# Optimization experiments

Measured on AMD Instinct MI355X. Metric: run time of the kernel, lower is better.

## Reference

```python
import jax, jax.numpy as jnp
import numpy as np

E = 128   # embed_dim / node feature width
H = 4     # num_heads
B = 512   # number of graphs
N = 65536 # total nodes


def setup_inputs() -> dict:
    key = jax.random.key(0)
    ks = jax.random.split(key, 12)
    s = 1.0 / np.sqrt(E)
    batch = jnp.sort(jax.random.randint(ks[0], (N,), 0, B))
    return {
        "x": jax.random.normal(ks[1], (N, E), jnp.float32),
        "metal_x": jax.random.normal(ks[2], (B, E), jnp.float32),
        "batch": batch,
        "Wk": jax.random.normal(ks[3], (E, E), jnp.float32) * s,
        "bk": jnp.zeros((E,), jnp.float32),
        "Wq": jax.random.normal(ks[4], (E, E), jnp.float32) * s,
        "bq": jnp.zeros((E,), jnp.float32),
        "in_w": jax.random.normal(ks[5], (3 * E, E), jnp.float32) * s,
        "in_b": jnp.zeros((3 * E,), jnp.float32),
        "out_w": jax.random.normal(ks[6], (E, E), jnp.float32) * s,
        "out_b": jnp.zeros((E,), jnp.float32),
    }


def reference(x, metal_x, batch, Wk, bk, Wq, bq, in_w, in_b, out_w, out_b):
    n, e = x.shape
    b = metal_x.shape[0]
    nb = np.asarray(batch)
    counts_np = np.bincount(nb, minlength=b)            # nodes per graph
    L = int(counts_np.max()) + 1                        # +1 for metal token at pos 0
    counts = jnp.asarray(counts_np)
    offsets = jnp.asarray(np.concatenate([[0], np.cumsum(counts_np)[:-1]]))
    pos = jnp.arange(n) - offsets[batch] + 1            # within-graph slot (metal at 0)

    # pad_sequence: value [L, B, E], slot 0 = metal_x, slots 1.. = graph nodes
    value = jnp.zeros((L, b, e), x.dtype)
    value = value.at[pos, batch].set(x)
    value = value.at[0, jnp.arange(b)].set(metal_x)

    # FCNN key/query (single hidden linear + relu, no output head)
    k_in = jax.nn.relu(value @ Wk.T + bk)
    q_in = jax.nn.relu(value @ Wq.T + bq)

    # MultiheadAttention (batch_first=False): in_proj then per-head scaled dot-product
    hd = e // H
    q = (q_in @ in_w[:e].T + in_b[:e]).reshape(L, b, H, hd)
    k = (k_in @ in_w[e:2 * e].T + in_b[e:2 * e]).reshape(L, b, H, hd)
    v = (value @ in_w[2 * e:].T + in_b[2 * e:]).reshape(L, b, H, hd)

    scores = jnp.einsum("lbhd,mbhd->bhlm", q, k) * (hd ** -0.5)
    valid = jnp.arange(L)[None, :] < (counts + 1)[:, None]   # [B, L] key_padding mask
    scores = jnp.where(valid[:, None, None, :], scores, jnp.finfo(scores.dtype).min)
    attn = jax.nn.softmax(scores, axis=-1)
    ctx = jnp.einsum("bhlm,mbhd->lbhd", attn, v).reshape(L, b, e)
    out = ctx @ out_w.T + out_b

    x_out = out[pos, batch]      # packed node outputs [N, E]
    metal_out = out[0]           # metal token outputs [B, E]
    return x_out, metal_out
```

## Files before the change

### kernel.cpp

```cpp
#include <hip/hip_runtime.h>

#define E   128
#define HD  32
#define NB  512
#define NN  65536
#define TT  (NB + NN)
#define TE  ((size_t)TT * 128)

typedef __attribute__((ext_vector_type(8))) short short8;
typedef __attribute__((ext_vector_type(4))) float f32x4;

__device__ __forceinline__ const float* row_ptr(const float* base, const float* metal, int t) {
  return (t < NB) ? metal + (size_t)t * E : base + (size_t)(t - NB) * E;
}
__device__ __forceinline__ float* row_ptr_w(float* base, float* metal, int t) {
  return (t < NB) ? metal + (size_t)t * E : base + (size_t)(t - NB) * E;
}

__device__ __forceinline__ unsigned short f2bf_rne(float x) {
  unsigned u = __float_as_uint(x);
  return (unsigned short)((u + 0x7FFFu + ((u >> 16) & 1u)) >> 16);
}
__device__ __forceinline__ void split_bf(float x, unsigned short& h, unsigned short& l) {
  h = f2bf_rne(x);
  float hf = __uint_as_float(((unsigned)h) << 16);
  l = f2bf_rne(x - hf);
}

__global__ void k_starts(const int* __restrict__ batch, int* __restrict__ start) {
  int i = blockIdx.x * blockDim.x + threadIdx.x;
  if (i >= NN) return;
  int bi = batch[i];
  int bp = (i == 0) ? -1 : batch[i - 1];
  for (int b = bp + 1; b <= bi; ++b) start[b] = i;
  if (i == NN - 1)
    for (int b = bi + 1; b <= NB; ++b) start[b] = NN;
}

__global__ void k_seqmap(const int* __restrict__ batch, const int* __restrict__ start,
                         int* __restrict__ seqmap) {
  int t = blockIdx.x * 256 + threadIdx.x;
  if (t >= TT) return;
  seqmap[t] = (t < NB) ? (start[t] + t) : (t - NB + batch[t - NB] + 1);
}

__global__ void k_wconv(const float* __restrict__ Wq, const float* __restrict__ Wk,
                        const float* __restrict__ in_w, const float* __restrict__ out_w,
                        unsigned short* __restrict__ Wh, unsigned short* __restrict__ Wl) {
  int idx = blockIdx.x * 256 + threadIdx.x;
  int r = idx >> 7, c = idx & 127;
  float v;
  if (r < 128)      v = Wq[r * 128 + c];
  else if (r < 256) v = Wk[(r - 128) * 128 + c];
  else if (r < 640) v = in_w[(r - 256) * 128 + c];
  else              v = out_w[(r - 640) * 128 + c];
  unsigned short h, l;
  split_bf(v, h, l);
  Wh[idx] = h;
  Wl[idx] = l;
}

__global__ __launch_bounds__(256, 2)
void k_outproj(const float* __restrict__ Ax, const int* __restrict__ rowmap,
               const unsigned short* __restrict__ Wh, const unsigned short* __restrict__ Wl,
               const float* __restrict__ bias,
               float* __restrict__ Cx, float* __restrict__ Cm) {
  __shared__ char smem[40960];
  float (*Afl)[36] = (float (*)[36])smem;
  unsigned short (*WldsH)[40] = (unsigned short (*)[40])(smem + 20480);
  unsigned short (*WldsL)[40] = (unsigned short (*)[40])(smem + 30720);

  const int tid = threadIdx.x;
  const int wave = tid >> 6;
  const int lane = tid & 63;
  const int lrow = lane & 15;
  const int q = lane >> 4;
  const int t0 = blockIdx.x * 128;

  f32x4 acc[2][8];
  #pragma unroll
  for (int mt = 0; mt < 2; ++mt)
    #pragma unroll
    for (int nt = 0; nt < 8; ++nt) acc[mt][nt] = (f32x4){0.f, 0.f, 0.f, 0.f};

  for (int ks = 0; ks < 4; ++ks) {
    __syncthreads();
    #pragma unroll
    for (int u = 0; u < 4; ++u) {
      int e4 = tid + u * 256;
      int m = e4 >> 3, k4 = e4 & 7;
      const float* rp = Ax + (size_t)rowmap[t0 + m] * E;
      float4 v = ((const float4*)(rp + ks * 32))[k4];
      *(float4*)&Afl[m][k4 * 4] = v;
    }
    #pragma unroll
    for (int u = 0; u < 4; ++u) {
      int idx = tid + u * 256;
      int half = idx >> 9, rem = idx & 511;
      int j = rem >> 2, seg = rem & 3;
      const unsigned short* src = (half ? Wl : Wh) + j * 128 + ks * 32 + seg * 8;
      short8 v = *(const short8*)src;
      unsigned short* dst = (half ? &WldsL[j][seg * 8] : &WldsH[j][seg * 8]);
      *(short8*)dst = v;
    }
    __syncthreads();

    short8 ah[2], al[2];
    #pragma unroll
    for (int mt = 0; mt < 2; ++mt) {
      int m = wave * 32 + mt * 16 + lrow;
      float4 f0 = *(const float4*)&Afl[m][q * 8];
      float4 f1 = *(const float4*)&Afl[m][q * 8 + 4];
      unsigned short h, l;
      split_bf(f0.x, h, l); ah[mt][0] = (short)h; al[mt][0] = (short)l;
      split_bf(f0.y, h, l); ah[mt][1] = (short)h; al[mt][1] = (short)l;
      split_bf(f0.z, h, l); ah[mt][2] = (short)h; al[mt][2] = (short)l;
      split_bf(f0.w, h, l); ah[mt][3] = (short)h; al[mt][3] = (short)l;
      split_bf(f1.x, h, l); ah[mt][4] = (short)h; al[mt][4] = (short)l;
      split_bf(f1.y, h, l); ah[mt][5] = (short)h; al[mt][5] = (short)l;
      split_bf(f1.z, h, l); ah[mt][6] = (short)h; al[mt][6] = (short)l;
      split_bf(f1.w, h, l); ah[mt][7] = (short)h; al[mt][7] = (short)l;
    }

    #pragma unroll
    for (int nt = 0; nt < 8; ++nt) {
      int j = nt * 16 + lrow;
      short8 bh = *(const short8*)&WldsH[j][q * 8];
      short8 bl = *(const short8*)&WldsL[j][q * 8];
      #pragma unroll
      for (int mt = 0; mt < 2; ++mt) {
        acc[mt][nt] = __builtin_amdgcn_mfma_f32_16x16x32_bf16(ah[mt], bh, acc[mt][nt], 0, 0, 0);
        acc[mt][nt] = __builtin_amdgcn_mfma_f32_16x16x32_bf16(al[mt], bh, acc[mt][nt], 0, 0, 0);
        acc[mt][nt] = __builtin_amdgcn_mfma_f32_16x16x32_bf16(ah[mt], bl, acc[mt][nt], 0, 0, 0);
      }
    }
  }

  #pragma unroll
  for (int mt = 0; mt < 2; ++mt) {
    #pragma unroll
    for (int reg = 0; reg < 4; ++reg) {
      int t = t0 + wave * 32 + mt * 16 + q * 4 + reg;
      float* cp = row_ptr_w(Cx, Cm, t);
      #pragma unroll
      for (int nt = 0; nt < 8; ++nt) {
        int j = nt * 16 + lrow;
        cp[j] = acc[mt][nt][reg] + bias[j];
      }
    }
  }
}

__global__ __launch_bounds__(256, 2)
void k_mega(const float* __restrict__ x, const float* __restrict__ metal_x,
            const unsigned short* __restrict__ Wh, const unsigned short* __restrict__ Wl,
            const float* __restrict__ bq, const float* __restrict__ bk,
            const float* __restrict__ in_b, float scl2,
            unsigned short* __restrict__ Voh,
            unsigned short* __restrict__ Qsh, unsigned short* __restrict__ Qsl,
            unsigned short* __restrict__ Ksh, unsigned short* __restrict__ Ksl,
            const int* __restrict__ seqmap) {
  __shared__ char smem[40960];
  float (*Afl)[36] = (float (*)[36])smem;
  unsigned short (*WldsH)[40] = (unsigned short (*)[40])(smem + 18432);
  unsigned short (*WldsL)[40] = (unsigned short (*)[40])(smem + 28672);
  unsigned short (*AshH)[40] = (unsigned short (*)[40])smem;
  unsigned short (*AshL)[40] = (unsigned short (*)[40])(smem + 10240);
  unsigned short (*W2ldsH)[40] = (unsigned short (*)[40])(smem + 20480);
  unsigned short (*W2ldsL)[40] = (unsigned short (*)[40])(smem + 30720);

  const int tid = threadIdx.x;
  const int wave = tid >> 6;
  const int lane = tid & 63;
  const int lrow = lane & 15;
  const int q = lane >> 4;
  const int group = (int)(blockIdx.x % 3);
  const int t0 = (int)(blockIdx.x / 3) * 128;

  const int w1o = (group == 0) ? 0 : (group == 1) ? 128 * 128 : 512 * 128;
  const unsigned short* W1h = Wh + w1o;
  const unsigned short* W1l = Wl + w1o;

  f32x4 acc1[2][8];
  #pragma unroll
  for (int mt = 0; mt < 2; ++mt)
    #pragma unroll
    for (int nt = 0; nt < 8; ++nt) acc1[mt][nt] = (f32x4){0.f, 0.f, 0.f, 0.f};

  for (int ks = 0; ks < 4; ++ks) {
    __syncthreads();
    #pragma unroll
    for (int u = 0; u < 4; ++u) {
      int e4 = tid + u * 256;
      int m = e4 >> 3, k4 = e4 & 7;
      const float* rp = row_ptr(x, metal_x, t0 + m);
      float4 v = ((const float4*)(rp + ks * 32))[k4];
      *(float4*)&Afl[m][k4 * 4] = v;
    }
    #pragma unroll
    for (int u = 0; u < 4; ++u) {
      int idx = tid + u * 256;
      int half = idx >> 9, rem = idx & 511;
      int j = rem >> 2, seg = rem & 3;
      const unsigned short* src = (half ? W1l : W1h) + j * 128 + ks * 32 + seg * 8;
      short8 v = *(const short8*)src;
      unsigned short* dst = (half ? &WldsL[j][seg * 8] : &WldsH[j][seg * 8]);
      *(short8*)dst = v;
    }
    __syncthreads();

    short8 ah[2], al[2];
    #pragma unroll
    for (int mt = 0; mt < 2; ++mt) {
      int m = wave * 32 + mt * 16 + lrow;
      float4 f0 = *(const float4*)&Afl[m][q * 8];
      float4 f1 = *(const float4*)&Afl[m][q * 8 + 4];
      unsigned short h, l;
      split_bf(f0.x, h, l); ah[mt][0] = (short)h; al[mt][0] = (short)l;
      split_bf(f0.y, h, l); ah[mt][1] = (short)h; al[mt][1] = (short)l;
      split_bf(f0.z, h, l); ah[mt][2] = (short)h; al[mt][2] = (short)l;
      split_bf(f0.w, h, l); ah[mt][3] = (short)h; al[mt][3] = (short)l;
      split_bf(f1.x, h, l); ah[mt][4] = (short)h; al[mt][4] = (short)l;
      split_bf(f1.y, h, l); ah[mt][5] = (short)h; al[mt][5] = (short)l;
      split_bf(f1.z, h, l); ah[mt][6] = (short)h; al[mt][6] = (short)l;
      split_bf(f1.w, h, l); ah[mt][7] = (short)h; al[mt][7] = (short)l;
    }

    #pragma unroll
    for (int nt = 0; nt < 8; ++nt) {
      int j = nt * 16 + lrow;
      short8 bh = *(const short8*)&WldsH[j][q * 8];
      short8 bl = *(const short8*)&WldsL[j][q * 8];
      #pragma unroll
      for (int mt = 0; mt < 2; ++mt) {
        acc1[mt][nt] = __builtin_amdgcn_mfma_f32_16x16x32_bf16(ah[mt], bh, acc1[mt][nt], 0, 0, 0);
        acc1[mt][nt] = __builtin_amdgcn_mfma_f32_16x16x32_bf16(al[mt], bh, acc1[mt][nt], 0, 0, 0);
        acc1[mt][nt] = __builtin_amdgcn_mfma_f32_16x16x32_bf16(ah[mt], bl, acc1[mt][nt], 0, 0, 0);
      }
    }
  }

  if (group == 2) {
    const float* bv = in_b + 2 * E;
    #pragma unroll
    for (int mt = 0; mt < 2; ++mt)
      #pragma unroll
      for (int reg = 0; reg < 4; ++reg) {
        int t = t0 + wave * 32 + mt * 16 + q * 4 + reg;
        size_t ro = (size_t)seqmap[t] * 128;
        #pragma unroll
        for (int nt = 0; nt < 8; ++nt) {
          int j = nt * 16 + lrow;
          Voh[ro + j] = f2bf_rne(acc1[mt][nt][reg] + bv[j]);
        }
      }
    return;
  }

  const int w2o = (group == 0) ? 256 * 128 : 384 * 128;
  const unsigned short* W2h = Wh + w2o;
  const unsigned short* W2l = Wl + w2o;
  const float* b1 = (group == 0) ? bq : bk;
  const float* b2 = (group == 0) ? in_b : in_b + 128;
  const float postscale = (group == 0) ? scl2 : 1.f;
  unsigned short* Oh = (group == 0) ? Qsh : Ksh;
  unsigned short* Ol = (group == 0) ? Qsl : Ksl;

  f32x4 acc2[2][8];
  #pragma unroll
  for (int mt = 0; mt < 2; ++mt)
    #pragma unroll
    for (int nt = 0; nt < 8; ++nt) acc2[mt][nt] = (f32x4){0.f, 0.f, 0.f, 0.f};

  float b1v[8];
  #pragma unroll
  for (int nt = 0; nt < 8; ++nt) b1v[nt] = b1[nt * 16 + lrow];

  #pragma unroll
  for (int ks2 = 0; ks2 < 4; ++ks2) {
    __syncthreads();
    #pragma unroll
    for (int u = 0; u < 4; ++u) {
      int idx = tid + u * 256;
      int half = idx >> 9, rem = idx & 511;
      int j = rem >> 2, seg = rem & 3;
      const unsigned short* src = (half ? W2l : W2h) + j * 128 + ks2 * 32 + seg * 8;
      short8 v = *(const short8*)src;
      unsigned short* dst = (half ? &W2ldsL[j][seg * 8] : &W2ldsH[j][seg * 8]);
      *(short8*)dst = v;
    }
    #pragma unroll
    for (int mt = 0; mt < 2; ++mt) {
      #pragma unroll
      for (int n2 = 0; n2 < 2; ++n2) {
        const int nt = ks2 * 2 + n2;
        #pragma unroll
        for (int reg = 0; reg < 4; ++reg) {
          int row = wave * 32 + mt * 16 + q * 4 + reg;
          float v = fmaxf(acc1[mt][nt][reg] + b1v[nt], 0.f);
          unsigned short h, l;
          split_bf(v, h, l);
          AshH[row][n2 * 16 + lrow] = h;
          AshL[row][n2 * 16 + lrow] = l;
        }
      }
    }
    __syncthreads();

    short8 ah[2], al[2];
    #pragma unroll
    for (int mt = 0; mt < 2; ++mt) {
      int m = wave * 32 + mt * 16 + lrow;
      ah[mt] = *(const short8*)&AshH[m][q * 8];
      al[mt] = *(const short8*)&AshL[m][q * 8];
    }
    #pragma unroll
    for (int nt = 0; nt < 8; ++nt) {
      int j = nt * 16 + lrow;
      short8 bh = *(const short8*)&W2ldsH[j][q * 8];
      short8 bl = *(const short8*)&W2ldsL[j][q * 8];
      #pragma unroll
      for (int mt = 0; mt < 2; ++mt) {
        acc2[mt][nt] = __builtin_amdgcn_mfma_f32_16x16x32_bf16(ah[mt], bh, acc2[mt][nt], 0, 0, 0);
        acc2[mt][nt] = __builtin_amdgcn_mfma_f32_16x16x32_bf16(al[mt], bh, acc2[mt][nt], 0, 0, 0);
        acc2[mt][nt] = __builtin_amdgcn_mfma_f32_16x16x32_bf16(ah[mt], bl, acc2[mt][nt], 0, 0, 0);
      }
    }
  }

  #pragma unroll
  for (int mt = 0; mt < 2; ++mt)
    #pragma unroll
    for (int reg = 0; reg < 4; ++reg) {
      int t = t0 + wave * 32 + mt * 16 + q * 4 + reg;
      size_t ro = (size_t)seqmap[t] * 128;
      #pragma unroll
      for (int nt = 0; nt < 8; ++nt) {
        int j = nt * 16 + lrow;
        float v = (acc2[mt][nt][reg] + b2[j]) * postscale;
        unsigned short h, l;
        split_bf(v, h, l);
        Oh[ro + j] = h;
        Ol[ro + j] = l;
      }
    }
}

__global__ __launch_bounds__(256, 4)
void k_flash(const unsigned short* __restrict__ Qh, const unsigned short* __restrict__ Ql,
             const unsigned short* __restrict__ Kh, const unsigned short* __restrict__ Kl,
             const unsigned short* __restrict__ Vb, const int* __restrict__ start,
             float* __restrict__ ctx) {
  __shared__ unsigned short Vlds[32][134];
  __shared__ alignas(16) unsigned PtH[4][32][20];
  __shared__ alignas(16) unsigned PtL[4][32][20];
  const int g = blockIdx.x;
  const int tid = threadIdx.x;
  const int wv = tid >> 6;
  const int lane = tid & 63;
  const int lrow = lane & 15;
  const int quad = lane >> 4;
  const int s0 = start[g];
  const int c = start[g + 1] - s0 + 1;
  const int sbase = s0 + g;
  const int hoff = wv * 32 + quad * 8;

  for (int qb = 32 * blockIdx.y; qb < c; qb += 32 * gridDim.y) {
    short8 qfh[2], qfl[2];
    #pragma unroll
    for (int mt = 0; mt < 2; ++mt) {
      int qs = qb + mt * 16 + lrow; if (qs >= c) qs = 0;
      size_t off = (size_t)(sbase + qs) * 128 + hoff;
      qfh[mt] = *(const short8*)(Qh + off);
      qfl[mt] = *(const short8*)(Ql + off);
    }
    float mr[2], lr[2];
    f32x4 O[2][2];
    #pragma unroll
    for (int mt = 0; mt < 2; ++mt) {
      mr[mt] = -3.0e38f; lr[mt] = 0.f;
      O[mt][0] = (f32x4){0.f, 0.f, 0.f, 0.f};
      O[mt][1] = (f32x4){0.f, 0.f, 0.f, 0.f};
    }

    const int nch = (c + 31) >> 5;
    for (int ch = 0; ch < nch; ++ch) {
      const int kb = ch * 32;
      short8 kfh[2], kfl[2];
      #pragma unroll
      for (int s = 0; s < 2; ++s) {
        int ks = kb + s * 16 + lrow; if (ks >= c) ks = 0;
        size_t off = (size_t)(sbase + ks) * 128 + hoff;
        kfh[s] = *(const short8*)(Kh + off);
        kfl[s] = *(const short8*)(Kl + off);
      }
      __syncthreads();
      #pragma unroll
      for (int r = 0; r < 2; ++r) {
        int key = r * 16 + (tid >> 4);
        int seg = tid & 15;
        int ks = kb + key; if (ks >= c) ks = 0;
        uint4 v = *(const uint4*)(Vb + (size_t)(sbase + ks) * 128 + seg * 8);
        unsigned* dst = (unsigned*)&Vlds[key][seg * 8];
        dst[0] = v.x; dst[1] = v.y; dst[2] = v.z; dst[3] = v.w;
      }
      __syncthreads();

      f32x4 sv[2][2];
      #pragma unroll
      for (int mt = 0; mt < 2; ++mt)
        #pragma unroll
        for (int s = 0; s < 2; ++s) {
          f32x4 z = (f32x4){0.f, 0.f, 0.f, 0.f};
          z = __builtin_amdgcn_mfma_f32_16x16x32_bf16(kfh[s], qfh[mt], z, 0, 0, 0);
          z = __builtin_amdgcn_mfma_f32_16x16x32_bf16(kfl[s], qfh[mt], z, 0, 0, 0);
          z = __builtin_amdgcn_mfma_f32_16x16x32_bf16(kfh[s], qfl[mt], z, 0, 0, 0);
          sv[mt][s] = z;
        }

      #pragma unroll
      for (int mt = 0; mt < 2; ++mt) {
        float m8 = mr[mt];
        #pragma unroll
        for (int s = 0; s < 2; ++s)
          #pragma unroll
          for (int r4 = 0; r4 < 4; ++r4) {
            bool valid = (kb + s * 16 + quad * 4 + r4) < c;
            float v = valid ? sv[mt][s][r4] : -3.0e38f;
            sv[mt][s][r4] = v;
            m8 = fmaxf(m8, v);
          }
        m8 = fmaxf(m8, __shfl_xor(m8, 16));
        m8 = fmaxf(m8, __shfl_xor(m8, 32));
        float al = exp2f(mr[mt] - m8);
        mr[mt] = m8;

        float p[2][4];
        float rs = 0.f;
        #pragma unroll
        for (int s = 0; s < 2; ++s)
          #pragma unroll
          for (int r4 = 0; r4 < 4; ++r4) {
            p[s][r4] = exp2f(sv[mt][s][r4] - m8);
            rs += p[s][r4];
          }
        rs += __shfl_xor(rs, 16);
        rs += __shfl_xor(rs, 32);
        lr[mt] = lr[mt] * al + rs;

        const int Q = mt * 16 + lrow;
        #pragma unroll
        for (int s = 0; s < 2; ++s) {
          unsigned short h0, l0, h1, l1, h2, l2, h3, l3;
          split_bf(p[s][0], h0, l0); split_bf(p[s][1], h1, l1);
          split_bf(p[s][2], h2, l2); split_bf(p[s][3], h3, l3);
          uint2 hw, lw;
          hw.x = (unsigned)h0 | ((unsigned)h1 << 16);
          hw.y = (unsigned)h2 | ((unsigned)h3 << 16);
          lw.x = (unsigned)l0 | ((unsigned)l1 << 16);
          lw.y = (unsigned)l2 | ((unsigned)l3 << 16);
          *(uint2*)&PtH[wv][Q][s * 8 + quad * 2] = hw;
          *(uint2*)&PtL[wv][Q][s * 8 + quad * 2] = lw;
        }
        #pragma unroll
        for (int nt = 0; nt < 2; ++nt)
          #pragma unroll
          for (int r4 = 0; r4 < 4; ++r4)
            O[mt][nt][r4] *= al;
      }

      short8 vf[2];
      #pragma unroll
      for (int nt = 0; nt < 2; ++nt)
        #pragma unroll
        for (int jj = 0; jj < 8; ++jj)
          vf[nt][jj] = (short)Vlds[quad * 8 + jj][wv * 32 + nt * 16 + lrow];

      #pragma unroll
      for (int mt = 0; mt < 2; ++mt) {
        short8 bh = *(const short8*)&PtH[wv][mt * 16 + lrow][quad * 4];
        short8 bl = *(const short8*)&PtL[wv][mt * 16 + lrow][quad * 4];
        #pragma unroll
        for (int nt = 0; nt < 2; ++nt) {
          O[mt][nt] = __builtin_amdgcn_mfma_f32_16x16x32_bf16(vf[nt], bh, O[mt][nt], 0, 0, 0);
          O[mt][nt] = __builtin_amdgcn_mfma_f32_16x16x32_bf16(vf[nt], bl, O[mt][nt], 0, 0, 0);
        }
      }
    }

    #pragma unroll
    for (int mt = 0; mt < 2; ++mt) {
      int qs = qb + mt * 16 + lrow;
      if (qs < c) {
        float inv = 1.f / lr[mt];
        float* cp = ctx + (size_t)(sbase + qs) * 128 + wv * 32 + quad * 4;
        float4 o0, o1;
        o0.x = O[mt][0][0] * inv; o0.y = O[mt][0][1] * inv;
        o0.z = O[mt][0][2] * inv; o0.w = O[mt][0][3] * inv;
        o1.x = O[mt][1][0] * inv; o1.y = O[mt][1][1] * inv;
        o1.z = O[mt][1][2] * inv; o1.w = O[mt][1][3] * inv;
        *(float4*)cp = o0;
        *(float4*)(cp + 16) = o1;
      }
    }
  }
}

extern "C" void kernel_launch(void* const* d_in, const int* in_sizes, int n_in,
                              void* d_out, int out_size, void* d_ws, size_t ws_size,
                              hipStream_t stream) {
  const float* x       = (const float*)d_in[0];
  const float* metal_x = (const float*)d_in[1];
  const int*   batch   = (const int*)d_in[2];
  const float* Wk      = (const float*)d_in[3];
  const float* bk      = (const float*)d_in[4];
  const float* Wq      = (const float*)d_in[5];
  const float* bq      = (const float*)d_in[6];
  const float* in_w    = (const float*)d_in[7];
  const float* in_b    = (const float*)d_in[8];
  const float* out_w   = (const float*)d_in[9];
  const float* out_b   = (const float*)d_in[10];
  float* out = (float*)d_out;

  float* ws = (float*)d_ws;
  int* start  = (int*)d_ws;
  int* seqmap = (int*)(ws + 528);
  unsigned short* Wh = (unsigned short*)(ws + 66576);
  unsigned short* Wl = Wh + 768 * 128;
  const size_t BUF0 = 164880;
  float* ctx = ws + BUF0;
  unsigned short* Qsh = (unsigned short*)(ws + BUF0 + TE);
  unsigned short* Qsl = Qsh + TE;
  unsigned short* Ksh = (unsigned short*)(ws + BUF0 + 2 * TE);
  unsigned short* Ksl = Ksh + TE;
  unsigned short* Vsb = (unsigned short*)(ws + BUF0 + 3 * TE);

  k_starts<<<NN / 256, 256, 0, stream>>>(batch, start);
  k_seqmap<<<TT / 256, 256, 0, stream>>>(batch, start, seqmap);
  k_wconv<<<768 * 128 / 256, 256, 0, stream>>>(Wq, Wk, in_w, out_w, Wh, Wl);

  const int gb = TT / 128;
  const float SCL2 = 0.17677669529663687f * 1.4426950408889634f;

  k_mega<<<gb * 3, 256, 0, stream>>>(
      x, metal_x, Wh, Wl, bq, bk, in_b, SCL2,
      Vsb, Qsh, Qsl, Ksh, Ksl, seqmap);

  dim3 agrid(NB, 6);
  k_flash<<<agrid, 256, 0, stream>>>(Qsh, Qsl, Ksh, Ksl, Vsb, start, ctx);

  k_outproj<<<gb, 256, 0, stream>>>(
      ctx, seqmap, Wh + 640 * 128, Wl + 640 * 128,
      out_b, out, out + (size_t)NN * E);
}
```

Measured before the change: 219.0 us.

## Fuse output projection into flash attention epilogue, dropping ctx buffer and kernel

The attention kernel now normalizes its context tile, splits it into bf16 hi/lo in shared memory, and runs the output projection GEMM per 32-query tile. It writes final outputs directly through a new inverse sequence map built in k_seqmap. This removes the fp32 ctx round trip through global memory and one kernel launch. In exchange, every query tile reloads the 128x128 out_w from L2, adds extra block barriers, uses more shared memory (40KB), and scatters stores at 4-byte granularity.

Result: slower. 244.9 us (+11.8%).

```diff
diff --git a/kernel.cpp b/kernel.cpp
--- a/kernel.cpp
+++ b/kernel.cpp
@@ -38,10 +38,12 @@
 }
 
 __global__ void k_seqmap(const int* __restrict__ batch, const int* __restrict__ start,
-                         int* __restrict__ seqmap) {
+                         int* __restrict__ seqmap, int* __restrict__ invmap) {
   int t = blockIdx.x * 256 + threadIdx.x;
   if (t >= TT) return;
-  seqmap[t] = (t < NB) ? (start[t] + t) : (t - NB + batch[t - NB] + 1);
+  int s = (t < NB) ? (start[t] + t) : (t - NB + batch[t - NB] + 1);
+  seqmap[t] = s;
+  invmap[s] = t;
 }
 
 __global__ void k_wconv(const float* __restrict__ Wq, const float* __restrict__ Wk,
@@ -58,97 +60,6 @@
   split_bf(v, h, l);
   Wh[idx] = h;
   Wl[idx] = l;
-}
-
-__global__ __launch_bounds__(256, 2)
-void k_outproj(const float* __restrict__ Ax, const int* __restrict__ rowmap,
-               const unsigned short* __restrict__ Wh, const unsigned short* __restrict__ Wl,
-               const float* __restrict__ bias,
-               float* __restrict__ Cx, float* __restrict__ Cm) {
-  __shared__ char smem[40960];
-  float (*Afl)[36] = (float (*)[36])smem;
-  unsigned short (*WldsH)[40] = (unsigned short (*)[40])(smem + 20480);
-  unsigned short (*WldsL)[40] = (unsigned short (*)[40])(smem + 30720);
-
-  const int tid = threadIdx.x;
-  const int wave = tid >> 6;
-  const int lane = tid & 63;
-  const int lrow = lane & 15;
-  const int q = lane >> 4;
-  const int t0 = blockIdx.x * 128;
-
-  f32x4 acc[2][8];
-  #pragma unroll
-  for (int mt = 0; mt < 2; ++mt)
-    #pragma unroll
-    for (int nt = 0; nt < 8; ++nt) acc[mt][nt] = (f32x4){0.f, 0.f, 0.f, 0.f};
-
-  for (int ks = 0; ks < 4; ++ks) {
-    __syncthreads();
-    #pragma unroll
-    for (int u = 0; u < 4; ++u) {
-      int e4 = tid + u * 256;
-      int m = e4 >> 3, k4 = e4 & 7;
-      const float* rp = Ax + (size_t)rowmap[t0 + m] * E;
-      float4 v = ((const float4*)(rp + ks * 32))[k4];
-      *(float4*)&Afl[m][k4 * 4] = v;
-    }
-    #pragma unroll
-    for (int u = 0; u < 4; ++u) {
-      int idx = tid + u * 256;
-      int half = idx >> 9, rem = idx & 511;
-      int j = rem >> 2, seg = rem & 3;
-      const unsigned short* src = (half ? Wl : Wh) + j * 128 + ks * 32 + seg * 8;
-      short8 v = *(const short8*)src;
-      unsigned short* dst = (half ? &WldsL[j][seg * 8] : &WldsH[j][seg * 8]);
-      *(short8*)dst = v;
-    }
-    __syncthreads();
-
-    short8 ah[2], al[2];
-    #pragma unroll
-    for (int mt = 0; mt < 2; ++mt) {
-      int m = wave * 32 + mt * 16 + lrow;
-      float4 f0 = *(const float4*)&Afl[m][q * 8];
-      float4 f1 = *(const float4*)&Afl[m][q * 8 + 4];
-      unsigned short h, l;
-      split_bf(f0.x, h, l); ah[mt][0] = (short)h; al[mt][0] = (short)l;
-      split_bf(f0.y, h, l); ah[mt][1] = (short)h; al[mt][1] = (short)l;
-      split_bf(f0.z, h, l); ah[mt][2] = (short)h; al[mt][2] = (short)l;
-      split_bf(f0.w, h, l); ah[mt][3] = (short)h; al[mt][3] = (short)l;
-      split_bf(f1.x, h, l); ah[mt][4] = (short)h; al[mt][4] = (short)l;
-      split_bf(f1.y, h, l); ah[mt][5] = (short)h; al[mt][5] = (short)l;
-      split_bf(f1.z, h, l); ah[mt][6] = (short)h; al[mt][6] = (short)l;
-      split_bf(f1.w, h, l); ah[mt][7] = (short)h; al[mt][7] = (short)l;
-    }
-
-    #pragma unroll
-    for (int nt = 0; nt < 8; ++nt) {
-      int j = nt * 16 + lrow;
-      short8 bh = *(const short8*)&WldsH[j][q * 8];
-      short8 bl = *(const short8*)&WldsL[j][q * 8];
-      #pragma unroll
-      for (int mt = 0; mt < 2; ++mt) {
-        acc[mt][nt] = __builtin_amdgcn_mfma_f32_16x16x32_bf16(ah[mt], bh, acc[mt][nt], 0, 0, 0);
-        acc[mt][nt] = __builtin_amdgcn_mfma_f32_16x16x32_bf16(al[mt], bh, acc[mt][nt], 0, 0, 0);
-        acc[mt][nt] = __builtin_amdgcn_mfma_f32_16x16x32_bf16(ah[mt], bl, acc[mt][nt], 0, 0, 0);
-      }
-    }
-  }
-
-  #pragma unroll
-  for (int mt = 0; mt < 2; ++mt) {
-    #pragma unroll
-    for (int reg = 0; reg < 4; ++reg) {
-      int t = t0 + wave * 32 + mt * 16 + q * 4 + reg;
-      float* cp = row_ptr_w(Cx, Cm, t);
-      #pragma unroll
-      for (int nt = 0; nt < 8; ++nt) {
-        int j = nt * 16 + lrow;
-        cp[j] = acc[mt][nt][reg] + bias[j];
-      }
-    }
-  }
 }
 
 __global__ __launch_bounds__(256, 2)
@@ -350,10 +261,18 @@
 void k_flash(const unsigned short* __restrict__ Qh, const unsigned short* __restrict__ Ql,
              const unsigned short* __restrict__ Kh, const unsigned short* __restrict__ Kl,
              const unsigned short* __restrict__ Vb, const int* __restrict__ start,
-             float* __restrict__ ctx) {
-  __shared__ unsigned short Vlds[32][134];
-  __shared__ alignas(16) unsigned PtH[4][32][20];
-  __shared__ alignas(16) unsigned PtL[4][32][20];
+             const unsigned short* __restrict__ Woh, const unsigned short* __restrict__ Wol,
+             const float* __restrict__ ob, const int* __restrict__ invmap,
+             float* __restrict__ outx, float* __restrict__ outm) {
+  __shared__ alignas(16) char smem[40960];
+  unsigned short (*Vlds)[134] = (unsigned short (*)[134])smem;
+  unsigned short (*WoH)[40] = (unsigned short (*)[40])smem;
+  unsigned short (*WoL)[40] = (unsigned short (*)[40])(smem + 10240);
+  unsigned (*PtH)[32][20] = (unsigned (*)[32][20])(smem + 20480);
+  unsigned (*PtL)[32][20] = (unsigned (*)[32][20])(smem + 30720);
+  unsigned short (*AshH)[136] = (unsigned short (*)[136])(smem + 20480);
+  unsigned short (*AshL)[136] = (unsigned short (*)[136])(smem + 29184);
+
   const int g = blockIdx.x;
   const int tid = threadIdx.x;
   const int wv = tid >> 6;
@@ -488,21 +407,86 @@
       }
     }
 
-    #pragma unroll
-    for (int mt = 0; mt < 2; ++mt) {
-      int qs = qb + mt * 16 + lrow;
-      if (qs < c) {
-        float inv = 1.f / lr[mt];
-        float* cp = ctx + (size_t)(sbase + qs) * 128 + wv * 32 + quad * 4;
-        float4 o0, o1;
-        o0.x = O[mt][0][0] * inv; o0.y = O[mt][0][1] * inv;
-        o0.z = O[mt][0][2] * inv; o0.w = O[mt][0][3] * inv;
-        o1.x = O[mt][1][0] * inv; o1.y = O[mt][1][1] * inv;
-        o1.z = O[mt][1][2] * inv; o1.w = O[mt][1][3] * inv;
-        *(float4*)cp = o0;
-        *(float4*)(cp + 16) = o1;
-      }
-    }
+    __syncthreads();
+    #pragma unroll
+    for (int mt = 0; mt < 2; ++mt) {
+      const int Q = mt * 16 + lrow;
+      float inv = 1.f / lr[mt];
+      #pragma unroll
+      for (int nt = 0; nt < 2; ++nt) {
+        unsigned short h0, l0, h1, l1, h2, l2, h3, l3;
+        split_bf(O[mt][nt][0] * inv, h0, l0);
+        split_bf(O[mt][nt][1] * inv, h1, l1);
+        split_bf(O[mt][nt][2] * inv, h2, l2);
+        split_bf(O[mt][nt][3] * inv, h3, l3);
+        uint2 hw, lw;
+        hw.x = (unsigned)h0 | ((unsigned)h1 << 16);
+        hw.y = (unsigned)h2 | ((unsigned)h3 << 16);
+        lw.x = (unsigned)l0 | ((unsigned)l1 << 16);
+        lw.y = (unsigned)l2 | ((unsigned)l3 << 16);
+        int d = wv * 32 + nt * 16 + quad * 4;
+        *(uint2*)&AshH[Q][d] = hw;
+        *(uint2*)&AshL[Q][d] = lw;
+      }
+    }
+    __syncthreads();
+
+    f32x4 acc2[2][2];
+    #pragma unroll
+    for (int mt = 0; mt < 2; ++mt) {
+      acc2[mt][0] = (f32x4){0.f, 0.f, 0.f, 0.f};
+      acc2[mt][1] = (f32x4){0.f, 0.f, 0.f, 0.f};
+    }
+
+    #pragma unroll
+    for (int ks2 = 0; ks2 < 4; ++ks2) {
+      if (ks2) __syncthreads();
+      #pragma unroll
+      for (int u = 0; u < 4; ++u) {
+        int idx = tid + u * 256;
+        int half = idx >> 9, rem = idx & 511;
+        int j = rem >> 2, seg = rem & 3;
+        const unsigned short* src = (half ? Wol : Woh) + j * 128 + ks2 * 32 + seg * 8;
+        short8 v = *(const short8*)src;
+        unsigned short* dst = (half ? &WoL[j][seg * 8] : &WoH[j][seg * 8]);
+        *(short8*)dst = v;
+      }
+      __syncthreads();
+
+      short8 ah[2], al[2];
+      #pragma unroll
+      for (int mt = 0; mt < 2; ++mt) {
+        ah[mt] = *(const short8*)&AshH[mt * 16 + lrow][ks2 * 32 + quad * 8];
+        al[mt] = *(const short8*)&AshL[mt * 16 + lrow][ks2 * 32 + quad * 8];
+      }
+      #pragma unroll
+      for (int nt = 0; nt < 2; ++nt) {
+        int j = wv * 32 + nt * 16 + lrow;
+        short8 bh = *(const short8*)&WoH[j][quad * 8];
+        short8 bl = *(const short8*)&WoL[j][quad * 8];
+        #pragma unroll
+        for (int mt = 0; mt < 2; ++mt) {
+          acc2[mt][nt] = __builtin_amdgcn_mfma_f32_16x16x32_bf16(ah[mt], bh, acc2[mt][nt], 0, 0, 0);
+          acc2[mt][nt] = __builtin_amdgcn_mfma_f32_16x16x32_bf16(al[mt], bh, acc2[mt][nt], 0, 0, 0);
+          acc2[mt][nt] = __builtin_amdgcn_mfma_f32_16x16x32_bf16(ah[mt], bl, acc2[mt][nt], 0, 0, 0);
+        }
+      }
+    }
+
+    float b2v0 = ob[wv * 32 + lrow];
+    float b2v1 = ob[wv * 32 + 16 + lrow];
+    #pragma unroll
+    for (int mt = 0; mt < 2; ++mt)
+      #pragma unroll
+      for (int reg = 0; reg < 4; ++reg) {
+        int qs = qb + mt * 16 + quad * 4 + reg;
+        if (qs < c) {
+          int t = invmap[sbase + qs];
+          float* cp = row_ptr_w(outx, outm, t);
+          cp[wv * 32 + lrow]      = acc2[mt][0][reg] + b2v0;
+          cp[wv * 32 + 16 + lrow] = acc2[mt][1][reg] + b2v1;
+        }
+      }
   }
 }
 
@@ -528,7 +512,7 @@
   unsigned short* Wh = (unsigned short*)(ws + 66576);
   unsigned short* Wl = Wh + 768 * 128;
   const size_t BUF0 = 164880;
-  float* ctx = ws + BUF0;
+  int* invmap = (int*)(ws + BUF0);
   unsigned short* Qsh = (unsigned short*)(ws + BUF0 + TE);
   unsigned short* Qsl = Qsh + TE;
   unsigned short* Ksh = (unsigned short*)(ws + BUF0 + 2 * TE);
@@ -536,7 +520,7 @@
   unsigned short* Vsb = (unsigned short*)(ws + BUF0 + 3 * TE);
 
   k_starts<<<NN / 256, 256, 0, stream>>>(batch, start);
-  k_seqmap<<<TT / 256, 256, 0, stream>>>(batch, start, seqmap);
+  k_seqmap<<<TT / 256, 256, 0, stream>>>(batch, start, seqmap, invmap);
   k_wconv<<<768 * 128 / 256, 256, 0, stream>>>(Wq, Wk, in_w, out_w, Wh, Wl);
 
   const int gb = TT / 128;
@@ -547,9 +531,8 @@
       Vsb, Qsh, Qsl, Ksh, Ksl, seqmap);
 
   dim3 agrid(NB, 6);
-  k_flash<<<agrid, 256, 0, stream>>>(Qsh, Qsl, Ksh, Ksl, Vsb, start, ctx);
-
-  k_outproj<<<gb, 256, 0, stream>>>(
-      ctx, seqmap, Wh + 640 * 128, Wl + 640 * 128,
-      out_b, out, out + (size_t)NN * E);
-}
+  k_flash<<<agrid, 256, 0, stream>>>(
+      Qsh, Qsl, Ksh, Ksl, Vsb, start,
+      Wh + 640 * 128, Wl + 640 * 128, out_b, invmap,
+      out, out + (size_t)NN * E);
+}
```

## Process 64 queries per flash block to reuse K/V loads; merge setup kernels

Applied to the files above, without the earlier changes.

Each flash-attention block now handles 64 query rows (four m-tiles) per pass instead of 32, processed in two halves, so every K chunk and V tile staged into LDS is reused across twice as many queries. The y-grid drops from 6 to 3 to match. The start-index and weight-conversion kernels are merged into one launch to save launch overhead. The cost is more registers per thread for Q fragments and accumulators, possibly lower occupancy, and fewer blocks, which means less parallelism for small graphs.

Result: slower. 246.3 us (+12.5%).

```diff
diff --git a/kernel.cpp b/kernel.cpp
--- a/kernel.cpp
+++ b/kernel.cpp
@@ -27,14 +27,31 @@
   l = f2bf_rne(x - hf);
 }
 
-__global__ void k_starts(const int* __restrict__ batch, int* __restrict__ start) {
-  int i = blockIdx.x * blockDim.x + threadIdx.x;
-  if (i >= NN) return;
-  int bi = batch[i];
-  int bp = (i == 0) ? -1 : batch[i - 1];
-  for (int b = bp + 1; b <= bi; ++b) start[b] = i;
-  if (i == NN - 1)
-    for (int b = bi + 1; b <= NB; ++b) start[b] = NN;
+__global__ void k_setup(const int* __restrict__ batch, int* __restrict__ start,
+                        const float* __restrict__ Wq, const float* __restrict__ Wk,
+                        const float* __restrict__ in_w, const float* __restrict__ out_w,
+                        unsigned short* __restrict__ Wh, unsigned short* __restrict__ Wl) {
+  int b = blockIdx.x;
+  if (b < 256) {
+    int i = b * 256 + threadIdx.x;
+    int bi = batch[i];
+    int bp = (i == 0) ? -1 : batch[i - 1];
+    for (int g = bp + 1; g <= bi; ++g) start[g] = i;
+    if (i == NN - 1)
+      for (int g = bi + 1; g <= NB; ++g) start[g] = NN;
+  } else {
+    int idx = (b - 256) * 256 + threadIdx.x;
+    int r = idx >> 7, c = idx & 127;
+    float v;
+    if (r < 128)      v = Wq[r * 128 + c];
+    else if (r < 256) v = Wk[(r - 128) * 128 + c];
+    else if (r < 640) v = in_w[(r - 256) * 128 + c];
+    else              v = out_w[(r - 640) * 128 + c];
+    unsigned short h, l;
+    split_bf(v, h, l);
+    Wh[idx] = h;
+    Wl[idx] = l;
+  }
 }
 
 __global__ void k_seqmap(const int* __restrict__ batch, const int* __restrict__ start,
@@ -42,22 +59,6 @@
   int t = blockIdx.x * 256 + threadIdx.x;
   if (t >= TT) return;
   seqmap[t] = (t < NB) ? (start[t] + t) : (t - NB + batch[t - NB] + 1);
-}
-
-__global__ void k_wconv(const float* __restrict__ Wq, const float* __restrict__ Wk,
-                        const float* __restrict__ in_w, const float* __restrict__ out_w,
-                        unsigned short* __restrict__ Wh, unsigned short* __restrict__ Wl) {
-  int idx = blockIdx.x * 256 + threadIdx.x;
-  int r = idx >> 7, c = idx & 127;
-  float v;
-  if (r < 128)      v = Wq[r * 128 + c];
-  else if (r < 256) v = Wk[(r - 128) * 128 + c];
-  else if (r < 640) v = in_w[(r - 256) * 128 + c];
-  else              v = out_w[(r - 640) * 128 + c];
-  unsigned short h, l;
-  split_bf(v, h, l);
-  Wh[idx] = h;
-  Wl[idx] = l;
 }
 
 __global__ __launch_bounds__(256, 2)
@@ -365,19 +366,19 @@
   const int sbase = s0 + g;
   const int hoff = wv * 32 + quad * 8;
 
-  for (int qb = 32 * blockIdx.y; qb < c; qb += 32 * gridDim.y) {
-    short8 qfh[2], qfl[2];
-    #pragma unroll
-    for (int mt = 0; mt < 2; ++mt) {
+  for (int qb = 64 * blockIdx.y; qb < c; qb += 64 * gridDim.y) {
+    short8 qfh[4], qfl[4];
+    #pragma unroll
+    for (int mt = 0; mt < 4; ++mt) {
       int qs = qb + mt * 16 + lrow; if (qs >= c) qs = 0;
       size_t off = (size_t)(sbase + qs) * 128 + hoff;
       qfh[mt] = *(const short8*)(Qh + off);
       qfl[mt] = *(const short8*)(Ql + off);
     }
-    float mr[2], lr[2];
-    f32x4 O[2][2];
-    #pragma unroll
-    for (int mt = 0; mt < 2; ++mt) {
+    float mr[4], lr[4];
+    f32x4 O[4][2];
+    #pragma unroll
+    for (int mt = 0; mt < 4; ++mt) {
       mr[mt] = -3.0e38f; lr[mt] = 0.f;
       O[mt][0] = (f32x4){0.f, 0.f, 0.f, 0.f};
       O[mt][1] = (f32x4){0.f, 0.f, 0.f, 0.f};
@@ -406,69 +407,6 @@
       }
       __syncthreads();
 
-      f32x4 sv[2][2];
-      #pragma unroll
-      for (int mt = 0; mt < 2; ++mt)
-        #pragma unroll
-        for (int s = 0; s < 2; ++s) {
-          f32x4 z = (f32x4){0.f, 0.f, 0.f, 0.f};
-          z = __builtin_amdgcn_mfma_f32_16x16x32_bf16(kfh[s], qfh[mt], z, 0, 0, 0);
-          z = __builtin_amdgcn_mfma_f32_16x16x32_bf16(kfl[s], qfh[mt], z, 0, 0, 0);
-          z = __builtin_amdgcn_mfma_f32_16x16x32_bf16(kfh[s], qfl[mt], z, 0, 0, 0);
-          sv[mt][s] = z;
-        }
-
-      #pragma unroll
-      for (int mt = 0; mt < 2; ++mt) {
-        float m8 = mr[mt];
-        #pragma unroll
-        for (int s = 0; s < 2; ++s)
-          #pragma unroll
-          for (int r4 = 0; r4 < 4; ++r4) {
-            bool valid = (kb + s * 16 + quad * 4 + r4) < c;
-            float v = valid ? sv[mt][s][r4] : -3.0e38f;
-            sv[mt][s][r4] = v;
-            m8 = fmaxf(m8, v);
-          }
-        m8 = fmaxf(m8, __shfl_xor(m8, 16));
-        m8 = fmaxf(m8, __shfl_xor(m8, 32));
-        float al = exp2f(mr[mt] - m8);
-        mr[mt] = m8;
-
-        float p[2][4];
-        float rs = 0.f;
-        #pragma unroll
-        for (int s = 0; s < 2; ++s)
-          #pragma unroll
-          for (int r4 = 0; r4 < 4; ++r4) {
-            p[s][r4] = exp2f(sv[mt][s][r4] - m8);
-            rs += p[s][r4];
-          }
-        rs += __shfl_xor(rs, 16);
-        rs += __shfl_xor(rs, 32);
-        lr[mt] = lr[mt] * al + rs;
-
-        const int Q = mt * 16 + lrow;
-        #pragma unroll
-        for (int s = 0; s < 2; ++s) {
-          unsigned short h0, l0, h1, l1, h2, l2, h3, l3;
-          split_bf(p[s][0], h0, l0); split_bf(p[s][1], h1, l1);
-          split_bf(p[s][2], h2, l2); split_bf(p[s][3], h3, l3);
-          uint2 hw, lw;
-          hw.x = (unsigned)h0 | ((unsigned)h1 << 16);
-          hw.y = (unsigned)h2 | ((unsigned)h3 << 16);
-          lw.x = (unsigned)l0 | ((unsigned)l1 << 16);
-          lw.y = (unsigned)l2 | ((unsigned)l3 << 16);
-          *(uint2*)&PtH[wv][Q][s * 8 + quad * 2] = hw;
-          *(uint2*)&PtL[wv][Q][s * 8 + quad * 2] = lw;
-        }
-        #pragma unroll
-        for (int nt = 0; nt < 2; ++nt)
-          #pragma unroll
-          for (int r4 = 0; r4 < 4; ++r4)
-            O[mt][nt][r4] *= al;
-      }
-
       short8 vf[2];
       #pragma unroll
       for (int nt = 0; nt < 2; ++nt)
@@ -476,20 +414,90 @@
         for (int jj = 0; jj < 8; ++jj)
           vf[nt][jj] = (short)Vlds[quad * 8 + jj][wv * 32 + nt * 16 + lrow];
 
-      #pragma unroll
-      for (int mt = 0; mt < 2; ++mt) {
-        short8 bh = *(const short8*)&PtH[wv][mt * 16 + lrow][quad * 4];
-        short8 bl = *(const short8*)&PtL[wv][mt * 16 + lrow][quad * 4];
+      const bool kv0 = (kb + quad * 4 + 0) < c;
+
+      #pragma unroll
+      for (int h = 0; h < 2; ++h) {
+        f32x4 sv[2][2];
         #pragma unroll
-        for (int nt = 0; nt < 2; ++nt) {
-          O[mt][nt] = __builtin_amdgcn_mfma_f32_16x16x32_bf16(vf[nt], bh, O[mt][nt], 0, 0, 0);
-          O[mt][nt] = __builtin_amdgcn_mfma_f32_16x16x32_bf16(vf[nt], bl, O[mt][nt], 0, 0, 0);
+        for (int mt2 = 0; mt2 < 2; ++mt2)
+          #pragma unroll
+          for (int s = 0; s < 2; ++s) {
+            f32x4 z = (f32x4){0.f, 0.f, 0.f, 0.f};
+            z = __builtin_amdgcn_mfma_f32_16x16x32_bf16(kfh[s], qfh[h * 2 + mt2], z, 0, 0, 0);
+            z = __builtin_amdgcn_mfma_f32_16x16x32_bf16(kfl[s], qfh[h * 2 + mt2], z, 0, 0, 0);
+            z = __builtin_amdgcn_mfma_f32_16x16x32_bf16(kfh[s], qfl[h * 2 + mt2], z, 0, 0, 0);
+            sv[mt2][s] = z;
+          }
+        (void)kv0;
+
+        #pragma unroll
+        for (int mt2 = 0; mt2 < 2; ++mt2) {
+          const int mt = h * 2 + mt2;
+          float m8 = mr[mt];
+          #pragma unroll
+          for (int s = 0; s < 2; ++s)
+            #pragma unroll
+            for (int r4 = 0; r4 < 4; ++r4) {
+              bool valid = (kb + s * 16 + quad * 4 + r4) < c;
+              float v = valid ? sv[mt2][s][r4] : -3.0e38f;
+              sv[mt2][s][r4] = v;
+              m8 = fmaxf(m8, v);
+            }
+          m8 = fmaxf(m8, __shfl_xor(m8, 16));
+          m8 = fmaxf(m8, __shfl_xor(m8, 32));
+          float al = exp2f(mr[mt] - m8);
+          mr[mt] = m8;
+
+          float p[2][4];
+          float rs = 0.f;
+          #pragma unroll
+          for (int s = 0; s < 2; ++s)
+            #pragma unroll
+            for (int r4 = 0; r4 < 4; ++r4) {
+              p[s][r4] = exp2f(sv[mt2][s][r4] - m8);
+              rs += p[s][r4];
+            }
+          rs += __shfl_xor(rs, 16);
+          rs += __shfl_xor(rs, 32);
+          lr[mt] = lr[mt] * al + rs;
+
+          const int Q = mt2 * 16 + lrow;
+          #pragma unroll
+          for (int s = 0; s < 2; ++s) {
+            unsigned short h0, l0, h1, l1, h2, l2, h3, l3;
+            split_bf(p[s][0], h0, l0); split_bf(p[s][1], h1, l1);
+            split_bf(p[s][2], h2, l2); split_bf(p[s][3], h3, l3);
+            uint2 hw, lw;
+            hw.x = (unsigned)h0 | ((unsigned)h1 << 16);
+            hw.y = (unsigned)h2 | ((unsigned)h3 << 16);
+            lw.x = (unsigned)l0 | ((unsigned)l1 << 16);
+            lw.y = (unsigned)l2 | ((unsigned)l3 << 16);
+            *(uint2*)&PtH[wv][Q][s * 8 + quad * 2] = hw;
+            *(uint2*)&PtL[wv][Q][s * 8 + quad * 2] = lw;
+          }
+          #pragma unroll
+          for (int nt = 0; nt < 2; ++nt)
+            #pragma unroll
+            for (int r4 = 0; r4 < 4; ++r4)
+              O[mt][nt][r4] *= al;
         }
-      }
-    }
-
-    #pragma unroll
-    for (int mt = 0; mt < 2; ++mt) {
+
+        #pragma unroll
+        for (int mt2 = 0; mt2 < 2; ++mt2) {
+          short8 bh = *(const short8*)&PtH[wv][mt2 * 16 + lrow][quad * 4];
+          short8 bl = *(const short8*)&PtL[wv][mt2 * 16 + lrow][quad * 4];
+          #pragma unroll
+          for (int nt = 0; nt < 2; ++nt) {
+            O[h * 2 + mt2][nt] = __builtin_amdgcn_mfma_f32_16x16x32_bf16(vf[nt], bh, O[h * 2 + mt2][nt], 0, 0, 0);
+            O[h * 2 + mt2][nt] = __builtin_amdgcn_mfma_f32_16x16x32_bf16(vf[nt], bl, O[h * 2 + mt2][nt], 0, 0, 0);
+          }
+        }
+      }
+    }
+
+    #pragma unroll
+    for (int mt = 0; mt < 4; ++mt) {
       int qs = qb + mt * 16 + lrow;
       if (qs < c) {
         float inv = 1.f / lr[mt];
@@ -535,9 +543,8 @@
   unsigned short* Ksl = Ksh + TE;
   unsigned short* Vsb = (unsigned short*)(ws + BUF0 + 3 * TE);
 
-  k_starts<<<NN / 256, 256, 0, stream>>>(batch, start);
-  k_seqmap<<<TT / 256, 256, 0, stream>>>(batch, start, seqmap);
-  k_wconv<<<768 * 128 / 256, 256, 0, stream>>>(Wq, Wk, in_w, out_w, Wh, Wl);
+  k_setup<<<640, 256, 0, stream>>>(batch, start, Wq, Wk, in_w, out_w, Wh, Wl);
+  k_seqmap<<<TT / 256 + 1, 256, 0, stream>>>(batch, start, seqmap);
 
   const int gb = TT / 128;
   const float SCL2 = 0.17677669529663687f * 1.4426950408889634f;
@@ -546,7 +553,7 @@
       x, metal_x, Wh, Wl, bq, bk, in_b, SCL2,
       Vsb, Qsh, Qsl, Ksh, Ksl, seqmap);
 
-  dim3 agrid(NB, 6);
+  dim3 agrid(NB, 3);
   k_flash<<<agrid, 256, 0, stream>>>(Qsh, Qsl, Ksh, Ksl, Vsb, start, ctx);
 
   k_outproj<<<gb, 256, 0, stream>>>(
```
